# Kernel tuning notes

Measured on AMD Instinct MI355X. Metric: run time of the kernel, lower is better.

The kernel has to match this reference:

```python
import jax, jax.numpy as jnp
import numpy as np
import math

NUM_HEADS = 16
KEY_SIZE = 64
HIDDEN = 4096
EMBED = 1024
VOCAB = 32000
SEQ = 2048
LAYERS = 4


def rmsnorm(x):
    return x * jax.lax.rsqrt(jnp.mean(x * x, axis=-1, keepdims=True) + 1e-5)


def rope_buffers(seq, d):
    half = d // 2
    i = jnp.arange(d)
    offset = i % half
    scales = jnp.power(10000.0, (-2.0 / d) * offset.astype(jnp.float32))
    m = jnp.arange(seq, dtype=jnp.float32)
    angles = m[:, None] * scales[None, :]  # [S, D]
    cos = jnp.cos(angles)
    sin = jnp.sin(angles)
    sin = jnp.concatenate([-sin[:, :half], sin[:, half:]], axis=-1)
    return cos, sin


def rotate(x, cos, sin):
    # x: [B, H, S, D]; cos/sin: [S, D]
    half = KEY_SIZE // 2
    swapped = jnp.concatenate([x[..., half:], x[..., :half]], axis=-1)
    return cos[None, None] * x + sin[None, None] * swapped


def setup_inputs() -> dict:
    key = jax.random.key(0)
    ks = jax.random.split(key, 7)
    std = 0.02
    return {
        'tokens': jax.random.randint(ks[0], (1, SEQ), 0, VOCAB),
        'table': jax.random.normal(ks[1], (VOCAB, EMBED), jnp.float32) * std,
        'qkv_w': jax.random.normal(ks[2], (LAYERS, EMBED, 3 * NUM_HEADS * KEY_SIZE), jnp.float32) * std,
        'out_w': jax.random.normal(ks[3], (LAYERS, NUM_HEADS * KEY_SIZE, EMBED), jnp.float32) * std,
        'up_w': jax.random.normal(ks[4], (LAYERS, EMBED, 2 * HIDDEN), jnp.float32) * std,
        'down_w': jax.random.normal(ks[5], (LAYERS, HIDDEN, EMBED), jnp.float32) * std,
        'vocab_w': jax.random.normal(ks[6], (EMBED, VOCAB), jnp.float32) * std,
    }


def reference(tokens, table, qkv_w, out_w, up_w, down_w, vocab_w):
    B, S = tokens.shape
    H, D = NUM_HEADS, KEY_SIZE
    # module zeroes embedding row 0 each forward
    table = table.at[0].set(0.0)
    cos, sin = rope_buffers(S, D)
    causal = jnp.tril(jnp.ones((S, S), dtype=bool))  # context_size == S -> pure causal
    emb = table[tokens]  # [B, S, E]
    for l in range(LAYERS):
        # --- self attention ---
        normed = rmsnorm(emb)
        qkv = normed @ qkv_w[l]  # [B, S, 3HD]
        q, k, v = jnp.split(qkv, 3, axis=-1)
        q = q.reshape(B, S, H, D).transpose(0, 2, 1, 3)
        k = k.reshape(B, S, H, D).transpose(0, 2, 1, 3)
        v = v.reshape(B, S, H, D).transpose(0, 2, 1, 3)
        q = rotate(q, cos, sin)
        k = rotate(k, cos, sin)
        attn = jnp.einsum('bhqd,bhkd->bhqk', q, k) / math.sqrt(D)
        attn = jnp.where(causal[None, None], attn, -jnp.inf)
        attn = jax.nn.softmax(attn, axis=-1)
        out = jnp.einsum('bhqk,bhkd->bhqd', attn, v)
        out = out.transpose(0, 2, 1, 3).reshape(B, S, H * D)
        emb = emb + out @ out_w[l]
        # --- SwiGLU FFN ---
        normed = rmsnorm(emb)
        gate_up = normed @ up_w[l]
        gate, up = gate_up[..., :HIDDEN], gate_up[..., HIDDEN:]
        emb = emb + (up * jax.nn.silu(gate)) @ down_w[l]
    emb = rmsnorm(emb)
    logits = emb @ vocab_w  # [B, S, V]
    return logits
```

## Files before the change

kernel.cpp:

```cpp
#include <hip/hip_runtime.h>
#include <hip/hip_bf16.h>

typedef __attribute__((ext_vector_type(8))) short short8;
typedef __attribute__((ext_vector_type(4))) float f32x4;

__device__ __forceinline__ ushort f2bf(float f) {
  uint32_t u = __float_as_uint(f);
  uint32_t r = (u + 0x7FFFu + ((u >> 16) & 1u)) >> 16;
  return (ushort)r;
}
__device__ __forceinline__ float bf2f(ushort u) {
  return __uint_as_float(((uint32_t)u) << 16);
}

__device__ __forceinline__ void gload_lds16(const ushort* g, ushort* l) {
  __builtin_amdgcn_global_load_lds(
      (const __attribute__((address_space(1))) void*)g,
      (__attribute__((address_space(3))) void*)l, 16, 0, 0);
}

__device__ __forceinline__ f32x4 mfma16(short8 a, short8 b, f32x4 c) {
  return __builtin_amdgcn_mfma_f32_16x16x32_bf16(a, b, c, 0, 0, 0);
}

#define BAR() __builtin_amdgcn_s_barrier()
#define WAIT_LGKM()                                        \
  do {                                                     \
    asm volatile("s_waitcnt lgkmcnt(0)" ::: "memory");     \
    __builtin_amdgcn_sched_barrier(0);                     \
  } while (0)
#define WAIT_VM0()                                         \
  do {                                                     \
    asm volatile("s_waitcnt vmcnt(0)" ::: "memory");       \
    __builtin_amdgcn_sched_barrier(0);                     \
  } while (0)
#define WAIT_VM4()                                         \
  do {                                                     \
    asm volatile("s_waitcnt vmcnt(4)" ::: "memory");       \
    __builtin_amdgcn_sched_barrier(0);                     \
  } while (0)

__global__ __launch_bounds__(256)
void transpose_conv_kernel(const float* __restrict__ W, ushort* __restrict__ WT,
                           const int K, const int N, const int mode) {
  const size_t lofs = (size_t)blockIdx.z * K * N;
  W += lofs;
  WT += lofs;
  __shared__ float tile[64][65];
  const int n0 = blockIdx.x * 64;
  const int k0 = blockIdx.y * 64;
  const int t = threadIdx.x;
#pragma unroll
  for (int j = 0; j < 4; ++j) {
    const int idx = j * 1024 + t * 4;
    const int kk = idx >> 6, nn = idx & 63;
    *(float4*)&tile[kk][nn] = *(const float4*)&W[(size_t)(k0 + kk) * N + n0 + nn];
  }
  __syncthreads();
#pragma unroll
  for (int j = 0; j < 4; ++j) {
    const int idx = j * 1024 + t * 4;
    const int nn = idx >> 6, kk = idx & 63;
    int rr = n0 + nn;
    if (mode == 1) rr = (rr < 4096) ? (2 * rr) : (2 * (rr - 4096) + 1);
    ushort4 o;
    o.x = f2bf(tile[kk + 0][nn]);
    o.y = f2bf(tile[kk + 1][nn]);
    o.z = f2bf(tile[kk + 2][nn]);
    o.w = f2bf(tile[kk + 3][nn]);
    *(ushort4*)&WT[(size_t)rr * K + k0 + kk] = o;
  }
}

__global__ __launch_bounds__(256)
void sincos_kernel(float2* __restrict__ cstab) {
  const int idx = blockIdx.x * 256 + threadIdx.x;
  const int s = idx >> 5, o = idx & 31;
  const float freq = exp2f(-0.41524101186092029f * (float)o);
  const float a = (float)s * freq;
  cstab[idx] = make_float2(cosf(a), sinf(a));
}

__global__ __launch_bounds__(256)
void embed_norm_kernel(const int* __restrict__ tokens, const float* __restrict__ table,
                       float* __restrict__ emb, ushort* __restrict__ normed) {
  const int s = blockIdx.x, t = threadIdx.x;
  const int tok = tokens[s];
  float4 v = make_float4(0.f, 0.f, 0.f, 0.f);
  if (tok != 0) v = *(const float4*)&table[(size_t)tok * 1024 + t * 4];
  *(float4*)&emb[(size_t)s * 1024 + t * 4] = v;
  float ss = v.x * v.x + v.y * v.y + v.z * v.z + v.w * v.w;
#pragma unroll
  for (int off = 32; off; off >>= 1) ss += __shfl_xor(ss, off);
  __shared__ float red[4];
  if ((t & 63) == 0) red[t >> 6] = ss;
  __syncthreads();
  const float total = red[0] + red[1] + red[2] + red[3];
  const float sc = rsqrtf(total * (1.f / 1024.f) + 1e-5f);
  ushort4 o;
  o.x = f2bf(v.x * sc); o.y = f2bf(v.y * sc);
  o.z = f2bf(v.z * sc); o.w = f2bf(v.w * sc);
  *(ushort4*)&normed[(size_t)s * 1024 + t * 4] = o;
}

__global__ __launch_bounds__(256)
void rmsnorm_kernel(const float* __restrict__ x, ushort* __restrict__ out) {
  const int row = blockIdx.x, t = threadIdx.x;
  const float4 v = *(const float4*)&x[(size_t)row * 1024 + t * 4];
  float ss = v.x * v.x + v.y * v.y + v.z * v.z + v.w * v.w;
#pragma unroll
  for (int off = 32; off; off >>= 1) ss += __shfl_xor(ss, off);
  __shared__ float red[4];
  if ((t & 63) == 0) red[t >> 6] = ss;
  __syncthreads();
  const float total = red[0] + red[1] + red[2] + red[3];
  const float sc = rsqrtf(total * (1.f / 1024.f) + 1e-5f);
  ushort4 o;
  o.x = f2bf(v.x * sc); o.y = f2bf(v.y * sc);
  o.z = f2bf(v.z * sc); o.w = f2bf(v.w * sc);
  *(ushort4*)&out[(size_t)row * 1024 + t * 4] = o;
}

__global__ __launch_bounds__(512)
void attn_mfma_kernel(const ushort* __restrict__ qh, const ushort* __restrict__ kh,
                      const ushort* __restrict__ vt, float* __restrict__ wso,
                      float* __restrict__ wsml) {
  __shared__ ushort sQ[128 * 64];
  __shared__ ushort sK[64 * 64];
  __shared__ ushort sV[64 * 64];
  __shared__ ushort sP[8][1024];
  const int h = blockIdx.y;
  const int u = blockIdx.x;
  const int qt_raw = u >> 1, half = u & 1;
  const int qt = (h < 8) ? qt_raw : 15 - qt_raw;
  const int i0 = qt * 128;
  const int tid = threadIdx.x;
  const int w = tid >> 6, lane = tid & 63;
  const int llo = lane & 15, lhi = lane >> 4;
  const ushort* qg = qh + ((size_t)h * 2048 + i0) * 64;
  const ushort* kg = kh + (size_t)h * 2048 * 64;
  const ushort* vg = vt + (size_t)h * 64 * 2048;

#pragma unroll
  for (int j = 0; j < 2; ++j) {
    const int cb = j * 512 + w * 64;
    const int ch = cb + lane;
    const int row = ch >> 3, c = ch & 7;
    gload_lds16(qg + (size_t)row * 64 + ((c ^ (row & 7)) * 8), &sQ[cb * 8]);
  }
  __syncthreads();
  const int qrow = w * 16 + llo;
  const short8 qf0 = *(const short8*)&sQ[qrow * 64 + ((lhi ^ (qrow & 7)) * 8)];
  const short8 qf1 = *(const short8*)&sQ[qrow * 64 + (((4 + lhi) ^ (qrow & 7)) * 8)];
  const int wmax = i0 + w * 16 + 15;

  float m = -1e30f, lsum = 0.f;
  f32x4 o[4] = {};
  const int c0 = half ? (qt + 1) : 0;
  const int c1 = half ? (2 * qt + 2) : (qt + 1);
  for (int cb2 = c0; cb2 < c1; ++cb2) {
    const int kb = cb2 * 64;
    __syncthreads();
    {
      const int cb = w * 64;
      const int ch = cb + lane;
      const int row = ch >> 3, c = ch & 7;
      gload_lds16(kg + (size_t)(kb + row) * 64 + ((c ^ (row & 7)) * 8), &sK[cb * 8]);
      gload_lds16(vg + (size_t)row * 2048 + kb + ((c ^ (row & 7)) * 8), &sV[cb * 8]);
    }
    __syncthreads();

    if (kb > wmax) continue;

    f32x4 st[4] = {};
#pragma unroll
    for (int ck = 0; ck < 2; ++ck) {
      const short8 qf = ck ? qf1 : qf0;
#pragma unroll
      for (int f = 0; f < 4; ++f) {
        const int key = f * 16 + llo;
        const short8 kf = *(const short8*)&sK[key * 64 + (((ck * 4 + lhi) ^ (key & 7)) * 8)];
        st[f] = mfma16(kf, qf, st[f]);
      }
    }

    float pv[4][4];
    const bool edge = (kb + 63 > i0 + w * 16);
#pragma unroll
    for (int f = 0; f < 4; ++f)
#pragma unroll
      for (int r = 0; r < 4; ++r) {
        float x = st[f][r] * 0.125f;
        if (edge && (kb - i0 + f * 16 + lhi * 4 + r) > qrow) x = -1e30f;
        pv[f][r] = x;
      }
    float mr = pv[0][0];
#pragma unroll
    for (int f = 0; f < 4; ++f)
#pragma unroll
      for (int r = 0; r < 4; ++r) mr = fmaxf(mr, pv[f][r]);
    mr = fmaxf(mr, __shfl_xor(mr, 16));
    mr = fmaxf(mr, __shfl_xor(mr, 32));
    const float mnew = fmaxf(m, mr);
    const float scale = __expf(m - mnew);
    m = mnew;
    float rs = 0.f;
#pragma unroll
    for (int f = 0; f < 4; ++f)
#pragma unroll
      for (int r = 0; r < 4; ++r) {
        const float p = __expf(pv[f][r] - mnew);
        pv[f][r] = p;
        rs += p;
      }
    rs += __shfl_xor(rs, 16);
    rs += __shfl_xor(rs, 32);
    lsum = lsum * scale + rs;
    float scr[4];
#pragma unroll
    for (int r = 0; r < 4; ++r) scr[r] = __shfl(scale, lhi * 4 + r);
#pragma unroll
    for (int nn = 0; nn < 4; ++nn)
#pragma unroll
      for (int r = 0; r < 4; ++r) o[nn][r] *= scr[r];

    ushort* pw = sP[w];
#pragma unroll
    for (int f = 0; f < 4; ++f) {
      uint2 pk;
      pk.x = (uint)f2bf(pv[f][0]) | ((uint)f2bf(pv[f][1]) << 16);
      pk.y = (uint)f2bf(pv[f][2]) | ((uint)f2bf(pv[f][3]) << 16);
      *(uint2*)&pw[llo * 64 + ((f * 16 + lhi * 4) ^ ((llo & 7) << 3))] = pk;
    }
    const short8 pf0 = *(const short8*)&pw[llo * 64 + ((lhi ^ (llo & 7)) * 8)];
    const short8 pf1 = *(const short8*)&pw[llo * 64 + (((4 + lhi) ^ (llo & 7)) * 8)];

#pragma unroll
    for (int ck = 0; ck < 2; ++ck) {
      const short8 pf = ck ? pf1 : pf0;
#pragma unroll
      for (int nn = 0; nn < 4; ++nn) {
        const int drow = nn * 16 + llo;
        const short8 vf = *(const short8*)&sV[drow * 64 + (((ck * 4 + lhi) ^ (drow & 7)) * 8)];
        o[nn] = mfma16(pf, vf, o[nn]);
      }
    }
  }

#pragma unroll
  for (int nn = 0; nn < 4; ++nn)
#pragma unroll
    for (int r = 0; r < 4; ++r) {
      const int row = i0 + w * 16 + lhi * 4 + r;
      wso[((size_t)(half * 16 + h) * 2048 + row) * 64 + nn * 16 + llo] = o[nn][r];
    }
  if (lhi == 0) {
    const int row = i0 + w * 16 + llo;
    *(float2*)&wsml[((size_t)(half * 16 + h) * 2048 + row) * 2] = make_float2(m, lsum);
  }
}

__global__ __launch_bounds__(256)
void attn_merge_kernel(const float* __restrict__ wso, const float* __restrict__ wsml,
                       ushort* __restrict__ attn_out) {
  const int row = blockIdx.x;
  const int t = threadIdx.x;
  const int h = t >> 4, dg = t & 15;
  const float2 ml1 = *(const float2*)&wsml[((size_t)h * 2048 + row) * 2];
  const float2 ml2 = *(const float2*)&wsml[((size_t)(16 + h) * 2048 + row) * 2];
  const float m = fmaxf(ml1.x, ml2.x);
  const float w1 = __expf(ml1.x - m), w2 = __expf(ml2.x - m);
  const float inv = 1.f / (ml1.y * w1 + ml2.y * w2);
  const float4 o1 = *(const float4*)&wso[((size_t)h * 2048 + row) * 64 + dg * 4];
  const float4 o2 = *(const float4*)&wso[((size_t)(16 + h) * 2048 + row) * 64 + dg * 4];
  ushort4 o;
  o.x = f2bf((o1.x * w1 + o2.x * w2) * inv);
  o.y = f2bf((o1.y * w1 + o2.y * w2) * inv);
  o.z = f2bf((o1.z * w1 + o2.z * w2) * inv);
  o.w = f2bf((o1.w * w1 + o2.w * w2) * inv);
  *(ushort4*)&attn_out[(size_t)row * 1024 + h * 64 + dg * 4] = o;
}

template <int BM, int BN, int EPI>
__global__ __launch_bounds__(256)
void gemm_bt64_kernel(const ushort* __restrict__ A, const ushort* __restrict__ BT,
                      const float* __restrict__ addend, void* __restrict__ Cout,
                      const int M, const int N, const int K) {
  constexpr int WM = BM / 2, WN = BN / 2;
  constexpr int FM = WM / 16, FN = WN / 16;
  __shared__ ushort sA[BM * 64];
  __shared__ ushort sB[BN * 64];
  const int bm0 = blockIdx.y * BM;
  const int bn0 = blockIdx.x * BN;
  const int tid = threadIdx.x;
  const int wid = tid >> 6, lane = tid & 63;
  const int wr = wid >> 1, wc = wid & 1;
  const int lhi = lane >> 4, llo = lane & 15;
  f32x4 acc[FM][FN] = {};
  for (int kt = 0; kt < K; kt += 64) {
#pragma unroll
    for (int i = 0; i < BM * 8 / 256; ++i) {
      const int cb = i * 256 + wid * 64;
      const int ch = cb + lane;
      const int row = ch >> 3, c = ch & 7;
      gload_lds16(A + (size_t)(bm0 + row) * K + kt + ((c ^ (row & 7)) * 8),
                  sA + (size_t)cb * 8);
    }
#pragma unroll
    for (int i = 0; i < BN * 8 / 256; ++i) {
      const int cb = i * 256 + wid * 64;
      const int ch = cb + lane;
      const int row = ch >> 3, c = ch & 7;
      gload_lds16(BT + (size_t)(bn0 + row) * K + kt + ((c ^ (row & 7)) * 8),
                  sB + (size_t)cb * 8);
    }
    __syncthreads();
    short8 aF[FM][2], bF[FN][2];
#pragma unroll
    for (int mm = 0; mm < FM; ++mm) {
      const int row = wr * WM + mm * 16 + llo;
#pragma unroll
      for (int ks = 0; ks < 2; ++ks)
        aF[mm][ks] = *(const short8*)&sA[row * 64 + (((ks * 4 + lhi) ^ (row & 7)) * 8)];
    }
#pragma unroll
    for (int nn = 0; nn < FN; ++nn) {
      const int row = wc * WN + nn * 16 + llo;
#pragma unroll
      for (int ks = 0; ks < 2; ++ks)
        bF[nn][ks] = *(const short8*)&sB[row * 64 + (((ks * 4 + lhi) ^ (row & 7)) * 8)];
    }
#pragma unroll
    for (int mm = 0; mm < FM; ++mm)
#pragma unroll
      for (int nn = 0; nn < FN; ++nn)
#pragma unroll
        for (int ks = 0; ks < 2; ++ks)
          acc[mm][nn] = mfma16(aF[mm][ks], bF[nn][ks], acc[mm][nn]);
    __syncthreads();
  }
#pragma unroll
  for (int mm = 0; mm < FM; ++mm) {
#pragma unroll
    for (int nn = 0; nn < FN; ++nn) {
      const int col = bn0 + wc * WN + nn * 16 + llo;
#pragma unroll
      for (int r = 0; r < 4; ++r) {
        const int row = bm0 + wr * WM + mm * 16 + lhi * 4 + r;
        float v = acc[mm][nn][r];
        if constexpr (EPI == 1) v += addend[(size_t)row * N + col];
        ((float*)Cout)[(size_t)row * N + col] = v;
      }
    }
  }
}

__global__ __launch_bounds__(256)
void gemm_qkv_kernel(const ushort* __restrict__ A, const ushort* __restrict__ BT,
                     const float2* __restrict__ cstab, ushort* __restrict__ qh,
                     ushort* __restrict__ kh, ushort* __restrict__ vt, const int K) {
  constexpr int BM = 128, BN = 128, WM = 64, WN = 64, FM = 4, FN = 4;
  __shared__ ushort sA[BM * 64];
  __shared__ ushort sB[BN * 64];
  const int bm0 = blockIdx.y * BM;
  const int bn0 = blockIdx.x * BN;
  const int tid = threadIdx.x;
  const int wid = tid >> 6, lane = tid & 63;
  const int wr = wid >> 1, wc = wid & 1;
  const int lhi = lane >> 4, llo = lane & 15;
  f32x4 acc[FM][FN] = {};
  for (int kt = 0; kt < K; kt += 64) {
#pragma unroll
    for (int i = 0; i < 4; ++i) {
      const int cb = i * 256 + wid * 64;
      const int ch = cb + lane;
      const int row = ch >> 3, c = ch & 7;
      gload_lds16(A + (size_t)(bm0 + row) * K + kt + ((c ^ (row & 7)) * 8),
                  sA + (size_t)cb * 8);
    }
#pragma unroll
    for (int i = 0; i < 4; ++i) {
      const int cb = i * 256 + wid * 64;
      const int ch = cb + lane;
      const int row = ch >> 3, c = ch & 7;
      gload_lds16(BT + (size_t)(bn0 + row) * K + kt + ((c ^ (row & 7)) * 8),
                  sB + (size_t)cb * 8);
    }
    __syncthreads();
    short8 aF[FM][2], bF[FN][2];
#pragma unroll
    for (int mm = 0; mm < FM; ++mm) {
      const int row = wr * WM + mm * 16 + llo;
#pragma unroll
      for (int ks = 0; ks < 2; ++ks)
        aF[mm][ks] = *(const short8*)&sA[row * 64 + (((ks * 4 + lhi) ^ (row & 7)) * 8)];
    }
#pragma unroll
    for (int nn = 0; nn < FN; ++nn) {
      const int row = wc * WN + nn * 16 + llo;
#pragma unroll
      for (int ks = 0; ks < 2; ++ks)
        bF[nn][ks] = *(const short8*)&sB[row * 64 + (((ks * 4 + lhi) ^ (row & 7)) * 8)];
    }
#pragma unroll
    for (int mm = 0; mm < FM; ++mm)
#pragma unroll
      for (int nn = 0; nn < FN; ++nn)
#pragma unroll
        for (int ks = 0; ks < 2; ++ks)
          acc[mm][nn] = mfma16(aF[mm][ks], bF[nn][ks], acc[mm][nn]);
    __syncthreads();
  }
#pragma unroll
  for (int mm = 0; mm < FM; ++mm) {
    const int row_base = bm0 + wr * WM + mm * 16 + lhi * 4;
#pragma unroll
    for (int nn = 0; nn < FN; ++nn) {
      const int col = bn0 + wc * WN + nn * 16 + llo;
      const int part = col >> 10;
      const int hcol = col & 1023;
      const int h = hcol >> 6;
      const int d = hcol & 63;
      const int off = d & 31;
      if (part == 2) {
        ushort4 o;
        o.x = f2bf(acc[mm][nn][0]);
        o.y = f2bf(acc[mm][nn][1]);
        o.z = f2bf(acc[mm][nn][2]);
        o.w = f2bf(acc[mm][nn][3]);
        *(ushort4*)&vt[((size_t)h * 64 + d) * 2048 + row_base] = o;
      } else {
#pragma unroll
        for (int r = 0; r < 4; ++r) {
          const int row = row_base + r;
          const float v = acc[mm][nn][r];
          const float pt = acc[mm][nn ^ 2][r];
          const float2 cn = cstab[row * 32 + off];
          const float si = (d < 32) ? -cn.y : cn.y;
          const ushort o = f2bf(cn.x * v + si * pt);
          const size_t ho = ((size_t)h * 2048 + row) * 64 + d;
          if (part == 0) qh[ho] = o; else kh[ho] = o;
        }
      }
    }
  }
}

template <int EPI>
__global__ __launch_bounds__(512, 2)
void gemm8p_kernel(const ushort* __restrict__ A, const ushort* __restrict__ BT,
                   void* __restrict__ Cout,
                   const int M, const int N, const int K, const int nby) {
  extern __shared__ ushort smem[];
  const int nwg = gridDim.x;
  const int cpx = nwg >> 3;
  int id = blockIdx.x;
  id = (id & 7) * cpx + (id >> 3);
  const int by = id % nby, bx = id / nby;
  const int bm0 = by * 256, bn0 = bx * 256;
  const int tid = threadIdx.x;
  const int wid = tid >> 6, lane = tid & 63;
  const int wr = wid >> 2, wc = wid & 3;
  const int llo = lane & 15, lhi = lane >> 4;
  const ushort* gA = A + (size_t)bm0 * K;
  const ushort* gB = BT + (size_t)bn0 * K;

  auto stage = [&](ushort* dst, int kt) {
#pragma unroll
    for (int i = 0; i < 2; ++i) {
      const int cb = i * 512 + wid * 64;
      const int ch = cb + lane;
      const int row = ch >> 2, c = ch & 3;
      gload_lds16(gA + (size_t)row * K + kt + ((c ^ ((row >> 1) & 3)) * 8),
                  dst + (size_t)cb * 8);
    }
#pragma unroll
    for (int i = 0; i < 2; ++i) {
      const int cb = i * 512 + wid * 64;
      const int ch = cb + lane;
      const int row = ch >> 2, c = ch & 3;
      gload_lds16(gB + (size_t)row * K + kt + ((c ^ ((row >> 1) & 3)) * 8),
                  dst + 8192 + (size_t)cb * 8);
    }
  };

  f32x4 acc[8][4] = {};
  short8 aF[4], bF[4];

  const int nt = K >> 5;
  stage(smem, 0);
  stage(smem + 16384, 32);
  WAIT_VM4();
  BAR();

  int cs = 0;
  for (int t = 0; t < nt; ++t) {
    ushort* cA = smem + cs * 16384;
    ushort* cB = cA + 8192;
    int ss = cs + 2; if (ss >= 3) ss -= 3;
    const bool pf2 = (t + 2 < nt);
    if (pf2) stage(smem + ss * 16384, (t + 2) * 32);
#pragma unroll
    for (int mm = 0; mm < 4; ++mm) {
      const int row = wr * 128 + mm * 16 + llo;
      aF[mm] = *(const short8*)&cA[row * 32 + ((lhi ^ ((row >> 1) & 3)) * 8)];
    }
#pragma unroll
    for (int nn = 0; nn < 4; ++nn) {
      const int row = wc * 64 + nn * 16 + llo;
      bF[nn] = *(const short8*)&cB[row * 32 + ((lhi ^ ((row >> 1) & 3)) * 8)];
    }
    BAR(); WAIT_LGKM();
    __builtin_amdgcn_s_setprio(1);
#pragma unroll
    for (int mm = 0; mm < 4; ++mm)
#pragma unroll
      for (int nn = 0; nn < 4; ++nn)
        acc[mm][nn] = mfma16(aF[mm], bF[nn], acc[mm][nn]);
    __builtin_amdgcn_s_setprio(0);
    BAR();
#pragma unroll
    for (int mm = 0; mm < 4; ++mm) {
      const int row = wr * 128 + (mm + 4) * 16 + llo;
      aF[mm] = *(const short8*)&cA[row * 32 + ((lhi ^ ((row >> 1) & 3)) * 8)];
    }
    BAR(); WAIT_LGKM();
    __builtin_amdgcn_s_setprio(1);
#pragma unroll
    for (int mm = 0; mm < 4; ++mm)
#pragma unroll
      for (int nn = 0; nn < 4; ++nn)
        acc[mm + 4][nn] = mfma16(aF[mm], bF[nn], acc[mm + 4][nn]);
    __builtin_amdgcn_s_setprio(0);
    if (pf2) { WAIT_VM4(); } else { WAIT_VM0(); }
    BAR();
    ++cs; if (cs == 3) cs = 0;
  }

#pragma unroll
  for (int m = 0; m < 8; ++m) {
#pragma unroll
    for (int n = 0; n < 4; ++n) {
      const int col = bn0 + wc * 64 + n * 16 + llo;
#pragma unroll
      for (int r = 0; r < 4; ++r) {
        const int row = bm0 + wr * 128 + m * 16 + lhi * 4 + r;
        float v = acc[m][n][r];
        if constexpr (EPI == 3) {
          const float other = __shfl_xor(v, 1);
          if ((llo & 1) == 0) {
            const float gate = v, up = other;
            const float hh = up * gate / (1.f + expf(-gate));
            ((ushort*)Cout)[(size_t)row * (N >> 1) + (col >> 1)] = f2bf(hh);
          }
        } else {
          ((float*)Cout)[(size_t)row * N + col] = v;
        }
      }
    }
  }
}

extern "C" void kernel_launch(void* const* d_in, const int* in_sizes, int n_in,
                              void* d_out, int out_size, void* d_ws, size_t ws_size,
                              hipStream_t stream) {
  const int* tokens    = (const int*)d_in[0];
  const float* table   = (const float*)d_in[1];
  const float* qkv_w   = (const float*)d_in[2];
  const float* out_w   = (const float*)d_in[3];
  const float* up_w    = (const float*)d_in[4];
  const float* down_w  = (const float*)d_in[5];
  const float* vocab_w = (const float*)d_in[6];
  float* logits = (float*)d_out;

  constexpr int G8P_LDS = 98304;
  hipFuncSetAttribute(reinterpret_cast<const void*>(&gemm8p_kernel<0>),
                      hipFuncAttributeMaxDynamicSharedMemorySize, G8P_LDS);
  hipFuncSetAttribute(reinterpret_cast<const void*>(&gemm8p_kernel<3>),
                      hipFuncAttributeMaxDynamicSharedMemorySize, G8P_LDS);

  char* p = (char*)d_ws;
  auto alloc = [&](size_t bytes) {
    char* r = p;
    p += (bytes + 255) & ~(size_t)255;
    return r;
  };
  float*  emb    = (float*)alloc(2048ull * 1024 * 4);
  ushort* normed = (ushort*)alloc(2048ull * 1024 * 2);
  float2* cstab  = (float2*)alloc(2048ull * 32 * 8);
  ushort* qhb    = (ushort*)alloc(16ull * 2048 * 64 * 2);
  ushort* khb    = (ushort*)alloc(16ull * 2048 * 64 * 2);
  ushort* vtb    = (ushort*)alloc(16ull * 64 * 2048 * 2);
  ushort* attno  = (ushort*)alloc(2048ull * 1024 * 2);
  float*  wso    = (float*)alloc(2ull * 16 * 2048 * 64 * 4);
  float*  wsml   = (float*)alloc(2ull * 16 * 2048 * 2 * 4);
  ushort* hbuf   = (ushort*)alloc(2048ull * 4096 * 2);
  ushort* qkvT   = (ushort*)alloc(4ull * 3072 * 1024 * 2);
  ushort* outT   = (ushort*)alloc(4ull * 1024 * 1024 * 2);
  ushort* upT    = (ushort*)alloc(4ull * 8192 * 1024 * 2);
  ushort* downT  = (ushort*)alloc(4ull * 1024 * 4096 * 2);
  ushort* vocabT = (ushort*)alloc(32000ull * 1024 * 2);

  transpose_conv_kernel<<<dim3(3072 / 64, 1024 / 64, 4), 256, 0, stream>>>(
      qkv_w, qkvT, 1024, 3072, 0);
  transpose_conv_kernel<<<dim3(1024 / 64, 1024 / 64, 4), 256, 0, stream>>>(
      out_w, outT, 1024, 1024, 0);
  transpose_conv_kernel<<<dim3(8192 / 64, 1024 / 64, 4), 256, 0, stream>>>(
      up_w, upT, 1024, 8192, 1);
  transpose_conv_kernel<<<dim3(1024 / 64, 4096 / 64, 4), 256, 0, stream>>>(
      down_w, downT, 4096, 1024, 0);
  transpose_conv_kernel<<<dim3(32000 / 64, 1024 / 64, 1), 256, 0, stream>>>(
      vocab_w, vocabT, 1024, 32000, 0);
  sincos_kernel<<<256, 256, 0, stream>>>(cstab);

  embed_norm_kernel<<<2048, 256, 0, stream>>>(tokens, table, emb, normed);

  for (int l = 0; l < 4; ++l) {
    if (l > 0) rmsnorm_kernel<<<2048, 256, 0, stream>>>(emb, normed);
    gemm_qkv_kernel<<<dim3(3072 / 128, 2048 / 128), 256, 0, stream>>>(
        normed, qkvT + (size_t)l * 3072 * 1024, cstab, qhb, khb, vtb, 1024);
    attn_mfma_kernel<<<dim3(32, 16), 512, 0, stream>>>(qhb, khb, vtb, wso, wsml);
    attn_merge_kernel<<<2048, 256, 0, stream>>>(wso, wsml, attno);
    gemm_bt64_kernel<64, 128, 1><<<dim3(1024 / 128, 2048 / 64), 256, 0, stream>>>(
        attno, outT + (size_t)l * 1024 * 1024, emb, emb, 2048, 1024, 1024);
    rmsnorm_kernel<<<2048, 256, 0, stream>>>(emb, normed);
    gemm8p_kernel<3><<<(8192 / 256) * (2048 / 256), 512, G8P_LDS, stream>>>(
        normed, upT + (size_t)l * 8192 * 1024, hbuf, 2048, 8192, 1024, 2048 / 256);
    gemm_bt64_kernel<64, 128, 1><<<dim3(1024 / 128, 2048 / 64), 256, 0, stream>>>(
        hbuf, downT + (size_t)l * 1024 * 4096, emb, emb, 2048, 1024, 4096);
  }
  rmsnorm_kernel<<<2048, 256, 0, stream>>>(emb, normed);
  gemm8p_kernel<0><<<(32000 / 256) * (2048 / 256), 512, G8P_LDS, stream>>>(
      normed, vocabT, logits, 2048, 32000, 1024, 2048 / 256);
}
```

Measured before the change: 1.205 ms.

## Fuse attention split-KV merge into the kernel with paired query-tile blocks

The attention kernel no longer splits each query tile's keys across two blocks whose partial results were merged by a separate kernel. Each block now processes two query tiles, u and 15-u, so every block does the same amount of causal work. It normalizes the output itself and writes bf16 directly to the attention output. This removes the merge launch and the fp32 partial-output and max/sum workspace traffic. In exchange the grid is halved to 256 blocks, which lowers concurrency per CU and lengthens the serial key loop in each block.

```diff
diff --git a/kernel.cpp b/kernel.cpp
--- a/kernel.cpp
+++ b/kernel.cpp
@@ -123,162 +123,142 @@
 
 __global__ __launch_bounds__(512)
 void attn_mfma_kernel(const ushort* __restrict__ qh, const ushort* __restrict__ kh,
-                      const ushort* __restrict__ vt, float* __restrict__ wso,
-                      float* __restrict__ wsml) {
+                      const ushort* __restrict__ vt, ushort* __restrict__ attn_out) {
   __shared__ ushort sQ[128 * 64];
   __shared__ ushort sK[64 * 64];
   __shared__ ushort sV[64 * 64];
   __shared__ ushort sP[8][1024];
   const int h = blockIdx.y;
   const int u = blockIdx.x;
-  const int qt_raw = u >> 1, half = u & 1;
-  const int qt = (h < 8) ? qt_raw : 15 - qt_raw;
-  const int i0 = qt * 128;
   const int tid = threadIdx.x;
   const int w = tid >> 6, lane = tid & 63;
   const int llo = lane & 15, lhi = lane >> 4;
-  const ushort* qg = qh + ((size_t)h * 2048 + i0) * 64;
   const ushort* kg = kh + (size_t)h * 2048 * 64;
   const ushort* vg = vt + (size_t)h * 64 * 2048;
 
-#pragma unroll
-  for (int j = 0; j < 2; ++j) {
-    const int cb = j * 512 + w * 64;
-    const int ch = cb + lane;
-    const int row = ch >> 3, c = ch & 7;
-    gload_lds16(qg + (size_t)row * 64 + ((c ^ (row & 7)) * 8), &sQ[cb * 8]);
-  }
-  __syncthreads();
-  const int qrow = w * 16 + llo;
-  const short8 qf0 = *(const short8*)&sQ[qrow * 64 + ((lhi ^ (qrow & 7)) * 8)];
-  const short8 qf1 = *(const short8*)&sQ[qrow * 64 + (((4 + lhi) ^ (qrow & 7)) * 8)];
-  const int wmax = i0 + w * 16 + 15;
-
-  float m = -1e30f, lsum = 0.f;
-  f32x4 o[4] = {};
-  const int c0 = half ? (qt + 1) : 0;
-  const int c1 = half ? (2 * qt + 2) : (qt + 1);
-  for (int cb2 = c0; cb2 < c1; ++cb2) {
-    const int kb = cb2 * 64;
-    __syncthreads();
-    {
-      const int cb = w * 64;
+  for (int seg = 0; seg < 2; ++seg) {
+    const int qt = seg ? (15 - u) : u;
+    const int i0 = qt * 128;
+    const ushort* qg = qh + ((size_t)h * 2048 + i0) * 64;
+
+#pragma unroll
+    for (int j = 0; j < 2; ++j) {
+      const int cb = j * 512 + w * 64;
       const int ch = cb + lane;
       const int row = ch >> 3, c = ch & 7;
-      gload_lds16(kg + (size_t)(kb + row) * 64 + ((c ^ (row & 7)) * 8), &sK[cb * 8]);
-      gload_lds16(vg + (size_t)row * 2048 + kb + ((c ^ (row & 7)) * 8), &sV[cb * 8]);
+      gload_lds16(qg + (size_t)row * 64 + ((c ^ (row & 7)) * 8), &sQ[cb * 8]);
     }
     __syncthreads();
-
-    if (kb > wmax) continue;
-
-    f32x4 st[4] = {};
-#pragma unroll
-    for (int ck = 0; ck < 2; ++ck) {
-      const short8 qf = ck ? qf1 : qf0;
+    const int qrow = w * 16 + llo;
+    const short8 qf0 = *(const short8*)&sQ[qrow * 64 + ((lhi ^ (qrow & 7)) * 8)];
+    const short8 qf1 = *(const short8*)&sQ[qrow * 64 + (((4 + lhi) ^ (qrow & 7)) * 8)];
+    const int wmax = i0 + w * 16 + 15;
+
+    float m = -1e30f, lsum = 0.f;
+    f32x4 o[4] = {};
+    const int nch = 2 * qt + 2;
+    for (int cb2 = 0; cb2 < nch; ++cb2) {
+      const int kb = cb2 * 64;
+      __syncthreads();
+      {
+        const int cb = w * 64;
+        const int ch = cb + lane;
+        const int row = ch >> 3, c = ch & 7;
+        gload_lds16(kg + (size_t)(kb + row) * 64 + ((c ^ (row & 7)) * 8), &sK[cb * 8]);
+        gload_lds16(vg + (size_t)row * 2048 + kb + ((c ^ (row & 7)) * 8), &sV[cb * 8]);
+      }
+      __syncthreads();
+
+      if (kb > wmax) continue;
+
+      f32x4 st[4] = {};
+#pragma unroll
+      for (int ck = 0; ck < 2; ++ck) {
+        const short8 qf = ck ? qf1 : qf0;
+#pragma unroll
+        for (int f = 0; f < 4; ++f) {
+          const int key = f * 16 + llo;
+          const short8 kf = *(const short8*)&sK[key * 64 + (((ck * 4 + lhi) ^ (key & 7)) * 8)];
+          st[f] = mfma16(kf, qf, st[f]);
+        }
+      }
+
+      float pv[4][4];
+      const bool edge = (kb + 63 > i0 + w * 16);
+#pragma unroll
+      for (int f = 0; f < 4; ++f)
+#pragma unroll
+        for (int r = 0; r < 4; ++r) {
+          float x = st[f][r] * 0.125f;
+          if (edge && (kb - i0 + f * 16 + lhi * 4 + r) > qrow) x = -1e30f;
+          pv[f][r] = x;
+        }
+      float mr = pv[0][0];
+#pragma unroll
+      for (int f = 0; f < 4; ++f)
+#pragma unroll
+        for (int r = 0; r < 4; ++r) mr = fmaxf(mr, pv[f][r]);
+      mr = fmaxf(mr, __shfl_xor(mr, 16));
+      mr = fmaxf(mr, __shfl_xor(mr, 32));
+      const float mnew = fmaxf(m, mr);
+      const float scale = __expf(m - mnew);
+      m = mnew;
+      float rs = 0.f;
+#pragma unroll
+      for (int f = 0; f < 4; ++f)
+#pragma unroll
+        for (int r = 0; r < 4; ++r) {
+          const float p = __expf(pv[f][r] - mnew);
+          pv[f][r] = p;
+          rs += p;
+        }
+      rs += __shfl_xor(rs, 16);
+      rs += __shfl_xor(rs, 32);
+      lsum = lsum * scale + rs;
+      float scr[4];
+#pragma unroll
+      for (int r = 0; r < 4; ++r) scr[r] = __shfl(scale, lhi * 4 + r);
+#pragma unroll
+      for (int nn = 0; nn < 4; ++nn)
+#pragma unroll
+        for (int r = 0; r < 4; ++r) o[nn][r] *= scr[r];
+
+      ushort* pw = sP[w];
 #pragma unroll
       for (int f = 0; f < 4; ++f) {
-        const int key = f * 16 + llo;
-        const short8 kf = *(const short8*)&sK[key * 64 + (((ck * 4 + lhi) ^ (key & 7)) * 8)];
-        st[f] = mfma16(kf, qf, st[f]);
-      }
-    }
-
-    float pv[4][4];
-    const bool edge = (kb + 63 > i0 + w * 16);
-#pragma unroll
-    for (int f = 0; f < 4; ++f)
+        uint2 pk;
+        pk.x = (uint)f2bf(pv[f][0]) | ((uint)f2bf(pv[f][1]) << 16);
+        pk.y = (uint)f2bf(pv[f][2]) | ((uint)f2bf(pv[f][3]) << 16);
+        *(uint2*)&pw[llo * 64 + ((f * 16 + lhi * 4) ^ ((llo & 7) << 3))] = pk;
+      }
+      const short8 pf0 = *(const short8*)&pw[llo * 64 + ((lhi ^ (llo & 7)) * 8)];
+      const short8 pf1 = *(const short8*)&pw[llo * 64 + (((4 + lhi) ^ (llo & 7)) * 8)];
+
+#pragma unroll
+      for (int ck = 0; ck < 2; ++ck) {
+        const short8 pf = ck ? pf1 : pf0;
+#pragma unroll
+        for (int nn = 0; nn < 4; ++nn) {
+          const int drow = nn * 16 + llo;
+          const short8 vf = *(const short8*)&sV[drow * 64 + (((ck * 4 + lhi) ^ (drow & 7)) * 8)];
+          o[nn] = mfma16(pf, vf, o[nn]);
+        }
+      }
+    }
+
+    const float inv = 1.f / lsum;
+    float invr[4];
+#pragma unroll
+    for (int r = 0; r < 4; ++r) invr[r] = __shfl(inv, lhi * 4 + r);
+#pragma unroll
+    for (int nn = 0; nn < 4; ++nn)
 #pragma unroll
       for (int r = 0; r < 4; ++r) {
-        float x = st[f][r] * 0.125f;
-        if (edge && (kb - i0 + f * 16 + lhi * 4 + r) > qrow) x = -1e30f;
-        pv[f][r] = x;
-      }
-    float mr = pv[0][0];
-#pragma unroll
-    for (int f = 0; f < 4; ++f)
-#pragma unroll
-      for (int r = 0; r < 4; ++r) mr = fmaxf(mr, pv[f][r]);
-    mr = fmaxf(mr, __shfl_xor(mr, 16));
-    mr = fmaxf(mr, __shfl_xor(mr, 32));
-    const float mnew = fmaxf(m, mr);
-    const float scale = __expf(m - mnew);
-    m = mnew;
-    float rs = 0.f;
-#pragma unroll
-    for (int f = 0; f < 4; ++f)
-#pragma unroll
-      for (int r = 0; r < 4; ++r) {
-        const float p = __expf(pv[f][r] - mnew);
-        pv[f][r] = p;
-        rs += p;
-      }
-    rs += __shfl_xor(rs, 16);
-    rs += __shfl_xor(rs, 32);
-    lsum = lsum * scale + rs;
-    float scr[4];
-#pragma unroll
-    for (int r = 0; r < 4; ++r) scr[r] = __shfl(scale, lhi * 4 + r);
-#pragma unroll
-    for (int nn = 0; nn < 4; ++nn)
-#pragma unroll
-      for (int r = 0; r < 4; ++r) o[nn][r] *= scr[r];
-
-    ushort* pw = sP[w];
-#pragma unroll
-    for (int f = 0; f < 4; ++f) {
-      uint2 pk;
-      pk.x = (uint)f2bf(pv[f][0]) | ((uint)f2bf(pv[f][1]) << 16);
-      pk.y = (uint)f2bf(pv[f][2]) | ((uint)f2bf(pv[f][3]) << 16);
-      *(uint2*)&pw[llo * 64 + ((f * 16 + lhi * 4) ^ ((llo & 7) << 3))] = pk;
-    }
-    const short8 pf0 = *(const short8*)&pw[llo * 64 + ((lhi ^ (llo & 7)) * 8)];
-    const short8 pf1 = *(const short8*)&pw[llo * 64 + (((4 + lhi) ^ (llo & 7)) * 8)];
-
-#pragma unroll
-    for (int ck = 0; ck < 2; ++ck) {
-      const short8 pf = ck ? pf1 : pf0;
-#pragma unroll
-      for (int nn = 0; nn < 4; ++nn) {
-        const int drow = nn * 16 + llo;
-        const short8 vf = *(const short8*)&sV[drow * 64 + (((ck * 4 + lhi) ^ (drow & 7)) * 8)];
-        o[nn] = mfma16(pf, vf, o[nn]);
-      }
-    }
-  }
-
-#pragma unroll
-  for (int nn = 0; nn < 4; ++nn)
-#pragma unroll
-    for (int r = 0; r < 4; ++r) {
-      const int row = i0 + w * 16 + lhi * 4 + r;
-      wso[((size_t)(half * 16 + h) * 2048 + row) * 64 + nn * 16 + llo] = o[nn][r];
-    }
-  if (lhi == 0) {
-    const int row = i0 + w * 16 + llo;
-    *(float2*)&wsml[((size_t)(half * 16 + h) * 2048 + row) * 2] = make_float2(m, lsum);
-  }
-}
-
-__global__ __launch_bounds__(256)
-void attn_merge_kernel(const float* __restrict__ wso, const float* __restrict__ wsml,
-                       ushort* __restrict__ attn_out) {
-  const int row = blockIdx.x;
-  const int t = threadIdx.x;
-  const int h = t >> 4, dg = t & 15;
-  const float2 ml1 = *(const float2*)&wsml[((size_t)h * 2048 + row) * 2];
-  const float2 ml2 = *(const float2*)&wsml[((size_t)(16 + h) * 2048 + row) * 2];
-  const float m = fmaxf(ml1.x, ml2.x);
-  const float w1 = __expf(ml1.x - m), w2 = __expf(ml2.x - m);
-  const float inv = 1.f / (ml1.y * w1 + ml2.y * w2);
-  const float4 o1 = *(const float4*)&wso[((size_t)h * 2048 + row) * 64 + dg * 4];
-  const float4 o2 = *(const float4*)&wso[((size_t)(16 + h) * 2048 + row) * 64 + dg * 4];
-  ushort4 o;
-  o.x = f2bf((o1.x * w1 + o2.x * w2) * inv);
-  o.y = f2bf((o1.y * w1 + o2.y * w2) * inv);
-  o.z = f2bf((o1.z * w1 + o2.z * w2) * inv);
-  o.w = f2bf((o1.w * w1 + o2.w * w2) * inv);
-  *(ushort4*)&attn_out[(size_t)row * 1024 + h * 64 + dg * 4] = o;
+        const int row = i0 + w * 16 + lhi * 4 + r;
+        attn_out[(size_t)row * 1024 + h * 64 + nn * 16 + llo] = f2bf(o[nn][r] * invr[r]);
+      }
+    __syncthreads();
+  }
 }
 
 template <int BM, int BN, int EPI>
@@ -592,8 +572,6 @@
   ushort* khb    = (ushort*)alloc(16ull * 2048 * 64 * 2);
   ushort* vtb    = (ushort*)alloc(16ull * 64 * 2048 * 2);
   ushort* attno  = (ushort*)alloc(2048ull * 1024 * 2);
-  float*  wso    = (float*)alloc(2ull * 16 * 2048 * 64 * 4);
-  float*  wsml   = (float*)alloc(2ull * 16 * 2048 * 2 * 4);
   ushort* hbuf   = (ushort*)alloc(2048ull * 4096 * 2);
   ushort* qkvT   = (ushort*)alloc(4ull * 3072 * 1024 * 2);
   ushort* outT   = (ushort*)alloc(4ull * 1024 * 1024 * 2);
@@ -619,8 +597,7 @@
     if (l > 0) rmsnorm_kernel<<<2048, 256, 0, stream>>>(emb, normed);
     gemm_qkv_kernel<<<dim3(3072 / 128, 2048 / 128), 256, 0, stream>>>(
         normed, qkvT + (size_t)l * 3072 * 1024, cstab, qhb, khb, vtb, 1024);
-    attn_mfma_kernel<<<dim3(32, 16), 512, 0, stream>>>(qhb, khb, vtb, wso, wsml);
-    attn_merge_kernel<<<2048, 256, 0, stream>>>(wso, wsml, attno);
+    attn_mfma_kernel<<<dim3(16, 16), 512, 0, stream>>>(qhb, khb, vtb, attno);
     gemm_bt64_kernel<64, 128, 1><<<dim3(1024 / 128, 2048 / 64), 256, 0, stream>>>(
         attno, outT + (size_t)l * 1024 * 1024, emb, emb, 2048, 1024, 1024);
     rmsnorm_kernel<<<2048, 256, 0, stream>>>(emb, normed);
```

Measured after the change: 1.287 ms. 1.07x slower.

## Double-buffer K/V tiles in attention kernel to overlap loads with compute

Applied to the files above, without the earlier changes.

The attention kernel now keeps two LDS buffers for K and V. It issues the async global-to-LDS load of the next key block before computing on the current one, replacing two barriers per iteration with one. The aim is to hide global load latency behind the QK^T, softmax and PV MFMA work. The cost is double the K/V shared memory, which may lower occupancy, and attention is only part of the full model's runtime.

```diff
diff --git a/kernel.cpp b/kernel.cpp
--- a/kernel.cpp
+++ b/kernel.cpp
@@ -126,8 +126,8 @@
                       const ushort* __restrict__ vt, float* __restrict__ wso,
                       float* __restrict__ wsml) {
   __shared__ ushort sQ[128 * 64];
-  __shared__ ushort sK[64 * 64];
-  __shared__ ushort sV[64 * 64];
+  __shared__ ushort sK[2][64 * 64];
+  __shared__ ushort sV[2][64 * 64];
   __shared__ ushort sP[8][1024];
   const int h = blockIdx.y;
   const int u = blockIdx.x;
@@ -141,6 +141,19 @@
   const ushort* kg = kh + (size_t)h * 2048 * 64;
   const ushort* vg = vt + (size_t)h * 64 * 2048;
 
+  const int scb = w * 64;
+  const int sch = scb + lane;
+  const int srow = sch >> 3, sc = sch & 7;
+  auto stage_kv = [&](int kb, int b) {
+    gload_lds16(kg + (size_t)(kb + srow) * 64 + ((sc ^ (srow & 7)) * 8),
+                &sK[b][scb * 8]);
+    gload_lds16(vg + (size_t)srow * 2048 + kb + ((sc ^ (srow & 7)) * 8),
+                &sV[b][scb * 8]);
+  };
+
+  const int c0 = half ? (qt + 1) : 0;
+  const int c1 = half ? (2 * qt + 2) : (qt + 1);
+
 #pragma unroll
   for (int j = 0; j < 2; ++j) {
     const int cb = j * 512 + w * 64;
@@ -148,6 +161,7 @@
     const int row = ch >> 3, c = ch & 7;
     gload_lds16(qg + (size_t)row * 64 + ((c ^ (row & 7)) * 8), &sQ[cb * 8]);
   }
+  stage_kv(c0 * 64, 0);
   __syncthreads();
   const int qrow = w * 16 + llo;
   const short8 qf0 = *(const short8*)&sQ[qrow * 64 + ((lhi ^ (qrow & 7)) * 8)];
@@ -156,95 +170,89 @@
 
   float m = -1e30f, lsum = 0.f;
   f32x4 o[4] = {};
-  const int c0 = half ? (qt + 1) : 0;
-  const int c1 = half ? (2 * qt + 2) : (qt + 1);
+  int bufc = 0;
   for (int cb2 = c0; cb2 < c1; ++cb2) {
     const int kb = cb2 * 64;
+    if (cb2 + 1 < c1) stage_kv((cb2 + 1) * 64, bufc ^ 1);
+
+    if (kb <= wmax) {
+      f32x4 st[4] = {};
+#pragma unroll
+      for (int ck = 0; ck < 2; ++ck) {
+        const short8 qf = ck ? qf1 : qf0;
+#pragma unroll
+        for (int f = 0; f < 4; ++f) {
+          const int key = f * 16 + llo;
+          const short8 kf = *(const short8*)&sK[bufc][key * 64 + (((ck * 4 + lhi) ^ (key & 7)) * 8)];
+          st[f] = mfma16(kf, qf, st[f]);
+        }
+      }
+
+      float pv[4][4];
+      const bool edge = (kb + 63 > i0 + w * 16);
+#pragma unroll
+      for (int f = 0; f < 4; ++f)
+#pragma unroll
+        for (int r = 0; r < 4; ++r) {
+          float x = st[f][r] * 0.125f;
+          if (edge && (kb - i0 + f * 16 + lhi * 4 + r) > qrow) x = -1e30f;
+          pv[f][r] = x;
+        }
+      float mr = pv[0][0];
+#pragma unroll
+      for (int f = 0; f < 4; ++f)
+#pragma unroll
+        for (int r = 0; r < 4; ++r) mr = fmaxf(mr, pv[f][r]);
+      mr = fmaxf(mr, __shfl_xor(mr, 16));
+      mr = fmaxf(mr, __shfl_xor(mr, 32));
+      const float mnew = fmaxf(m, mr);
+      const float scale = __expf(m - mnew);
+      m = mnew;
+      float rs = 0.f;
+#pragma unroll
+      for (int f = 0; f < 4; ++f)
+#pragma unroll
+        for (int r = 0; r < 4; ++r) {
+          const float p = __expf(pv[f][r] - mnew);
+          pv[f][r] = p;
+          rs += p;
+        }
+      rs += __shfl_xor(rs, 16);
+      rs += __shfl_xor(rs, 32);
+      lsum = lsum * scale + rs;
+      float scr[4];
+#pragma unroll
+      for (int r = 0; r < 4; ++r) scr[r] = __shfl(scale, lhi * 4 + r);
+#pragma unroll
+      for (int nn = 0; nn < 4; ++nn)
+#pragma unroll
+        for (int r = 0; r < 4; ++r) o[nn][r] *= scr[r];
+
+      ushort* pw = sP[w];
+#pragma unroll
+      for (int f = 0; f < 4; ++f) {
+        uint2 pk;
+        pk.x = (uint)f2bf(pv[f][0]) | ((uint)f2bf(pv[f][1]) << 16);
+        pk.y = (uint)f2bf(pv[f][2]) | ((uint)f2bf(pv[f][3]) << 16);
+        *(uint2*)&pw[llo * 64 + ((f * 16 + lhi * 4) ^ ((llo & 7) << 3))] = pk;
+      }
+      const short8 pf0 = *(const short8*)&pw[llo * 64 + ((lhi ^ (llo & 7)) * 8)];
+      const short8 pf1 = *(const short8*)&pw[llo * 64 + (((4 + lhi) ^ (llo & 7)) * 8)];
+
+#pragma unroll
+      for (int ck = 0; ck < 2; ++ck) {
+        const short8 pf = ck ? pf1 : pf0;
+#pragma unroll
+        for (int nn = 0; nn < 4; ++nn) {
+          const int drow = nn * 16 + llo;
+          const short8 vf = *(const short8*)&sV[bufc][drow * 64 + (((ck * 4 + lhi) ^ (drow & 7)) * 8)];
+          o[nn] = mfma16(pf, vf, o[nn]);
+        }
+      }
+    }
+
     __syncthreads();
-    {
-      const int cb = w * 64;
-      const int ch = cb + lane;
-      const int row = ch >> 3, c = ch & 7;
-      gload_lds16(kg + (size_t)(kb + row) * 64 + ((c ^ (row & 7)) * 8), &sK[cb * 8]);
-      gload_lds16(vg + (size_t)row * 2048 + kb + ((c ^ (row & 7)) * 8), &sV[cb * 8]);
-    }
-    __syncthreads();
-
-    if (kb > wmax) continue;
-
-    f32x4 st[4] = {};
-#pragma unroll
-    for (int ck = 0; ck < 2; ++ck) {
-      const short8 qf = ck ? qf1 : qf0;
-#pragma unroll
-      for (int f = 0; f < 4; ++f) {
-        const int key = f * 16 + llo;
-        const short8 kf = *(const short8*)&sK[key * 64 + (((ck * 4 + lhi) ^ (key & 7)) * 8)];
-        st[f] = mfma16(kf, qf, st[f]);
-      }
-    }
-
-    float pv[4][4];
-    const bool edge = (kb + 63 > i0 + w * 16);
-#pragma unroll
-    for (int f = 0; f < 4; ++f)
-#pragma unroll
-      for (int r = 0; r < 4; ++r) {
-        float x = st[f][r] * 0.125f;
-        if (edge && (kb - i0 + f * 16 + lhi * 4 + r) > qrow) x = -1e30f;
-        pv[f][r] = x;
-      }
-    float mr = pv[0][0];
-#pragma unroll
-    for (int f = 0; f < 4; ++f)
-#pragma unroll
-      for (int r = 0; r < 4; ++r) mr = fmaxf(mr, pv[f][r]);
-    mr = fmaxf(mr, __shfl_xor(mr, 16));
-    mr = fmaxf(mr, __shfl_xor(mr, 32));
-    const float mnew = fmaxf(m, mr);
-    const float scale = __expf(m - mnew);
-    m = mnew;
-    float rs = 0.f;
-#pragma unroll
-    for (int f = 0; f < 4; ++f)
-#pragma unroll
-      for (int r = 0; r < 4; ++r) {
-        const float p = __expf(pv[f][r] - mnew);
-        pv[f][r] = p;
-        rs += p;
-      }
-    rs += __shfl_xor(rs, 16);
-    rs += __shfl_xor(rs, 32);
-    lsum = lsum * scale + rs;
-    float scr[4];
-#pragma unroll
-    for (int r = 0; r < 4; ++r) scr[r] = __shfl(scale, lhi * 4 + r);
-#pragma unroll
-    for (int nn = 0; nn < 4; ++nn)
-#pragma unroll
-      for (int r = 0; r < 4; ++r) o[nn][r] *= scr[r];
-
-    ushort* pw = sP[w];
-#pragma unroll
-    for (int f = 0; f < 4; ++f) {
-      uint2 pk;
-      pk.x = (uint)f2bf(pv[f][0]) | ((uint)f2bf(pv[f][1]) << 16);
-      pk.y = (uint)f2bf(pv[f][2]) | ((uint)f2bf(pv[f][3]) << 16);
-      *(uint2*)&pw[llo * 64 + ((f * 16 + lhi * 4) ^ ((llo & 7) << 3))] = pk;
-    }
-    const short8 pf0 = *(const short8*)&pw[llo * 64 + ((lhi ^ (llo & 7)) * 8)];
-    const short8 pf1 = *(const short8*)&pw[llo * 64 + (((4 + lhi) ^ (llo & 7)) * 8)];
-
-#pragma unroll
-    for (int ck = 0; ck < 2; ++ck) {
-      const short8 pf = ck ? pf1 : pf0;
-#pragma unroll
-      for (int nn = 0; nn < 4; ++nn) {
-        const int drow = nn * 16 + llo;
-        const short8 vf = *(const short8*)&sV[drow * 64 + (((ck * 4 + lhi) ^ (drow & 7)) * 8)];
-        o[nn] = mfma16(pf, vf, o[nn]);
-      }
-    }
+    bufc ^= 1;
   }
 
 #pragma unroll
```

New measurement: 1.191 ms. No clear change (-1.2%).
